# Kernel tuning notes

Hardware: AMD Instinct MI355X
Metric: run time of the kernel (lower is better)

## Reference

```python
import jax, jax.numpy as jnp
import numpy as np

N, E, IN, HID, OUT, L = 50000, 800000, 128, 64, 40, 3


def setup_inputs() -> dict:
    key = jax.random.key(0)
    ks = jax.random.split(key, 10)
    x = jax.random.normal(ks[0], (N, IN), jnp.float32)
    edge_index = jax.random.randint(ks[1], (2, E), 0, N, dtype=jnp.int32)

    def u(k, shape, fan_in):
        s = 1.0 / np.sqrt(fan_in)
        return jax.random.uniform(k, shape, jnp.float32, -s, s)

    return {
        "x": x,
        "edge_index": edge_index,
        # former1 (NWGformerF): in -> hidden projection
        "Wf": u(ks[2], (IN, HID), IN),
        "bf": jnp.zeros((HID,), jnp.float32),
        # stacked GCNConv weights (hidden->hidden)
        "conv_W": u(ks[3], (L, HID, HID), HID),
        "conv_b": jnp.zeros((L, HID), jnp.float32),
        # residual linears
        "lin_W": u(ks[4], (L, HID, HID), HID),
        "lin_b": u(ks[5], (L, HID), HID),
        # batchnorm (eval mode: affine with running stats)
        "gamma": jnp.ones((L, HID), jnp.float32),
        "beta": jnp.zeros((L, HID), jnp.float32),
        "run_mean": jnp.zeros((L, HID), jnp.float32),
        "run_var": jnp.ones((L, HID), jnp.float32),
        # output head
        "pred_W": u(ks[6], (HID, OUT), HID),
        "pred_b": jnp.zeros((OUT,), jnp.float32),
    }


def reference(x, edge_index, Wf, bf, conv_W, conv_b, lin_W, lin_b,
              gamma, beta, run_mean, run_var, pred_W, pred_b):
    n = x.shape[0]
    src, dst = edge_index[0], edge_index[1]
    eps = 1e-5

    # GCN symmetric normalization with self-loops: deg over dst (+1 self loop)
    deg = jax.ops.segment_sum(jnp.ones(src.shape[0], x.dtype), dst,
                              num_segments=n) + 1.0
    dinv = jax.lax.rsqrt(deg)                      # [N]
    edge_coef = dinv[src] * dinv[dst]              # [E]
    self_coef = (dinv * dinv)[:, None]             # [N,1]

    def gcn(h, W, b):
        hw = h @ W                                 # [N,HID]
        agg = jax.ops.segment_sum(hw[src] * edge_coef[:, None], dst,
                                  num_segments=n)
        return agg + hw * self_coef + b

    # former1: in -> hidden (dropout is identity in eval mode)
    h = x @ Wf + bf

    for i in range(L):
        h = gcn(h, conv_W[i], conv_b[i]) + h @ lin_W[i] + lin_b[i]  # res
        h = (h - run_mean[i]) * (gamma[i] * jax.lax.rsqrt(run_var[i] + eps)) + beta[i]
        h = jax.nn.relu(h)

    return h @ pred_W + pred_b
```

## Files before the change

kernel.cpp:

```cpp
#include <hip/hip_runtime.h>
#include <hip/hip_bf16.h>
#include <hip/hip_fp16.h>

#define IN_DIM 128
#define HID 64
#define OUT_DIM 40
#define SPAD 68

typedef __hip_bfloat16 bf16;
typedef unsigned short u16;
typedef _Float16 f16;
typedef __attribute__((ext_vector_type(8))) _Float16 f16x8;
typedef __attribute__((ext_vector_type(4))) float f32x4;

__device__ __forceinline__ float b2f(bf16 v) { return __bfloat162float(v); }
__device__ __forceinline__ float relu_f(float x) { return 0.5f * (x + fabsf(x)); }
__device__ __forceinline__ float ldv(const void* p, int i, int is32) {
    return is32 ? ((const float*)p)[i] : b2f(((const bf16*)p)[i]);
}

__global__ void MPNNs_60198261620971_kernel() {}

__global__ void canary_k(float* out, int m) {
    int i = blockIdx.x * blockDim.x + threadIdx.x;
    if (i < m) out[i] = 1234.0f;
}


__global__ void zerodetect_k(unsigned int* __restrict__ c2r, int nw,
                             const unsigned int* __restrict__ rv, int* __restrict__ flag) {
    int i = blockIdx.x * blockDim.x + threadIdx.x;
    if (i < nw) c2r[i] = 0;
    if (i == 0) flag[0] = (rv[0] == 0x3F800000u) ? 1 : 0;
}

__global__ void count_k(const int* __restrict__ dst, unsigned int* __restrict__ c2r,
                        u16* __restrict__ rank, int e, int n, int n2) {
    int i = blockIdx.x * blockDim.x + threadIdx.x;
    if (i >= e) return;
    int xcc = __builtin_amdgcn_s_getreg((31u << 11) | 20) & 7;
    int d = dst[i];
    u16 r = 0;
    if ((unsigned)d < (unsigned)n) {
        int sh = (d & 1) * 16;
        unsigned old = atomicAdd(&c2r[(size_t)xcc * n2 + (d >> 1)], 1u << sh);
        r = (u16)(((old >> sh) & 0x1FFFu) | ((unsigned)xcc << 13));
    }
    rank[i] = r;
}

__global__ void scan1_k(const unsigned int* __restrict__ c2r, int* __restrict__ row_ptr,
                        int* __restrict__ psum, float* __restrict__ dinv,
                        u16* __restrict__ base, int n, int n2) {
    __shared__ int sdata[1024];
    int i = blockIdx.x * 1024 + threadIdx.x;
    int v = 0;
    if (i < n) {
        int sh = (i & 1) * 16;
        int acc = 0;
        u16 b[8];
        #pragma unroll
        for (int r = 0; r < 8; r++) {
            b[r] = (u16)acc;
            acc += (int)((c2r[(size_t)r * n2 + (i >> 1)] >> sh) & 0xFFFFu);
        }
        v = acc;
        uint4 bw;
        bw.x = (unsigned)b[0] | ((unsigned)b[1] << 16);
        bw.y = (unsigned)b[2] | ((unsigned)b[3] << 16);
        bw.z = (unsigned)b[4] | ((unsigned)b[5] << 16);
        bw.w = (unsigned)b[6] | ((unsigned)b[7] << 16);
        *(uint4*)&base[(size_t)i * 8] = bw;
        dinv[i] = rsqrtf((float)v + 1.0f);
    }
    sdata[threadIdx.x] = v;
    __syncthreads();
    for (int off = 1; off < 1024; off <<= 1) {
        int t = (threadIdx.x >= off) ? sdata[threadIdx.x - off] : 0;
        __syncthreads();
        sdata[threadIdx.x] += t;
        __syncthreads();
    }
    if (i < n) row_ptr[i] = sdata[threadIdx.x] - v;
    if (threadIdx.x == 1023) psum[blockIdx.x] = sdata[1023];
}

__global__ void scan2_k(int* __restrict__ psum, int* __restrict__ row_ptr, int nb, int n) {
    __shared__ int sdata[1024];
    int v = (threadIdx.x < nb) ? psum[threadIdx.x] : 0;
    sdata[threadIdx.x] = v;
    __syncthreads();
    for (int off = 1; off < 1024; off <<= 1) {
        int t = (threadIdx.x >= off) ? sdata[threadIdx.x - off] : 0;
        __syncthreads();
        sdata[threadIdx.x] += t;
        __syncthreads();
    }
    if (threadIdx.x < nb) psum[threadIdx.x] = sdata[threadIdx.x] - v;
    if (threadIdx.x == 1023) row_ptr[n] = sdata[1023];
}

__global__ void scan3_k(int* __restrict__ row_ptr, const int* __restrict__ psum, int n) {
    int i = blockIdx.x * blockDim.x + threadIdx.x;
    if (i < n) row_ptr[i] += psum[i >> 10];
}

__global__ void fill_k(const int* __restrict__ src, const int* __restrict__ dst,
                       const int* __restrict__ row_ptr, const u16* __restrict__ rank,
                       const u16* __restrict__ base, u16* __restrict__ col, int e, int n) {
    int i = blockIdx.x * blockDim.x + threadIdx.x;
    if (i < e) {
        int d = dst[i];
        if ((unsigned)d < (unsigned)n) {
            u16 rw = rank[i];
            int rep = rw >> 13, lr = rw & 0x1FFF;
            col[row_ptr[d] + (int)base[(size_t)d * 8 + rep] + lr] = (u16)src[i];
        }
    }
}


__global__ __launch_bounds__(256) void former_k(const void* __restrict__ x,
                                                const void* __restrict__ Wf,
                                                const void* __restrict__ bfv,
                                                const int* __restrict__ dflag,
                                                float* __restrict__ h, int n) {
    __shared__ float sW[IN_DIM * HID];
    __shared__ float sx[64 * SPAD];
    int is32 = dflag[0];
    if (is32) {
        const float4* w4 = (const float4*)Wf;
        for (int i = threadIdx.x; i < IN_DIM * HID / 4; i += 256) ((float4*)sW)[i] = w4[i];
    } else {
        for (int i = threadIdx.x; i < IN_DIM * HID; i += 256) sW[i] = b2f(((const bf16*)Wf)[i]);
    }
    int tid = threadIdx.x, cg = tid & 15, rg = tid >> 4;
    int rowBase = blockIdx.x * 64;
    float acc[4][4];
    #pragma unroll
    for (int i = 0; i < 4; i++)
        #pragma unroll
        for (int j = 0; j < 4; j++) acc[i][j] = 0.f;

    for (int p = 0; p < 2; p++) {
        __syncthreads();
        #pragma unroll
        for (int pass = 0; pass < 4; pass++) {
            int r = pass * 16 + (tid >> 4);
            int c = (tid & 15) * 4;
            int gr = rowBase + r;
            float4 v = make_float4(0.f, 0.f, 0.f, 0.f);
            if (gr < n) {
                if (is32) v = *(const float4*)((const float*)x + (size_t)gr * IN_DIM + p * 64 + c);
                else {
                    const bf16* xb = (const bf16*)x + (size_t)gr * IN_DIM + p * 64 + c;
                    v = make_float4(b2f(xb[0]), b2f(xb[1]), b2f(xb[2]), b2f(xb[3]));
                }
            }
            *(float4*)&sx[r * SPAD + c] = v;
        }
        __syncthreads();
        for (int k = 0; k < 64; k += 4) {
            float4 hr[4], w[4];
            #pragma unroll
            for (int i = 0; i < 4; i++) hr[i] = *(float4*)&sx[(rg * 4 + i) * SPAD + k];
            #pragma unroll
            for (int j = 0; j < 4; j++) w[j] = *(float4*)&sW[(p * 64 + k + j) * HID + cg * 4];
            #pragma unroll
            for (int i = 0; i < 4; i++) {
                const float* hh = (const float*)&hr[i];
                #pragma unroll
                for (int j = 0; j < 4; j++) {
                    const float* ww = (const float*)&w[j];
                    acc[i][0] += hh[j] * ww[0];
                    acc[i][1] += hh[j] * ww[1];
                    acc[i][2] += hh[j] * ww[2];
                    acc[i][3] += hh[j] * ww[3];
                }
            }
        }
    }
    float b0 = ldv(bfv, cg * 4 + 0, is32), b1 = ldv(bfv, cg * 4 + 1, is32);
    float b2 = ldv(bfv, cg * 4 + 2, is32), b3 = ldv(bfv, cg * 4 + 3, is32);
    #pragma unroll
    for (int i = 0; i < 4; i++) {
        int r = rowBase + rg * 4 + i;
        if (r < n) {
            float4 o = make_float4(acc[i][0] + b0, acc[i][1] + b1, acc[i][2] + b2, acc[i][3] + b3);
            *(float4*)&h[(size_t)r * HID + cg * 4] = o;
        }
    }
}

__global__ __launch_bounds__(256) void dense_k(float* __restrict__ h,
                                               const void* __restrict__ convW,
                                               const void* __restrict__ linW,
                                               const void* __restrict__ convB,
                                               const void* __restrict__ linB,
                                               const int* __restrict__ dflag,
                                               const float* __restrict__ dinv,
                                               __half* __restrict__ hws, int n, int l) {
    __shared__ __align__(16) f16 wT[2][HID][72];
    int is32 = dflag[0];
    int wOff = l * HID * HID, vOff = l * HID;
    for (int i = threadIdx.x; i < HID * HID; i += 256) {
        int k = i >> 6, nn = i & 63;
        wT[0][nn][k] = (f16)ldv(convW, wOff + i, is32);
        wT[1][nn][k] = (f16)ldv(linW, wOff + i, is32);
    }
    __syncthreads();
    int wave = threadIdx.x >> 6, lane = threadIdx.x & 63;
    int m = lane & 15, quad = lane >> 4;
    int row0 = blockIdx.x * 64 + wave * 16;
    if (row0 >= n) return;
    int ar = row0 + m;
    const float* hp = h + (size_t)((ar < n) ? ar : 0) * HID;
    float4 v0 = *(const float4*)(hp + quad * 8);
    float4 v1 = *(const float4*)(hp + quad * 8 + 4);
    float4 v2 = *(const float4*)(hp + 32 + quad * 8);
    float4 v3 = *(const float4*)(hp + 32 + quad * 8 + 4);
    f16x8 a0 = { (f16)v0.x, (f16)v0.y, (f16)v0.z, (f16)v0.w,
                 (f16)v1.x, (f16)v1.y, (f16)v1.z, (f16)v1.w };
    f16x8 a1 = { (f16)v2.x, (f16)v2.y, (f16)v2.z, (f16)v2.w,
                 (f16)v3.x, (f16)v3.y, (f16)v3.z, (f16)v3.w };
    f32x4 acc[2][4];
    #pragma unroll
    for (int t = 0; t < 2; t++)
        #pragma unroll
        for (int ct = 0; ct < 4; ct++) acc[t][ct] = (f32x4){0.f, 0.f, 0.f, 0.f};
    #pragma unroll
    for (int ct = 0; ct < 4; ct++) {
        int nn = ct * 16 + m;
        f16x8 b00 = *(const f16x8*)&wT[0][nn][quad * 8];
        f16x8 b01 = *(const f16x8*)&wT[0][nn][32 + quad * 8];
        f16x8 b10 = *(const f16x8*)&wT[1][nn][quad * 8];
        f16x8 b11 = *(const f16x8*)&wT[1][nn][32 + quad * 8];
        acc[0][ct] = __builtin_amdgcn_mfma_f32_16x16x32_f16(a0, b00, acc[0][ct], 0, 0, 0);
        acc[0][ct] = __builtin_amdgcn_mfma_f32_16x16x32_f16(a1, b01, acc[0][ct], 0, 0, 0);
        acc[1][ct] = __builtin_amdgcn_mfma_f32_16x16x32_f16(a0, b10, acc[1][ct], 0, 0, 0);
        acc[1][ct] = __builtin_amdgcn_mfma_f32_16x16x32_f16(a1, b11, acc[1][ct], 0, 0, 0);
    }
    float cbv[4];
    #pragma unroll
    for (int ct = 0; ct < 4; ct++)
        cbv[ct] = ldv(convB, vOff + ct * 16 + m, is32) + ldv(linB, vOff + ct * 16 + m, is32);
    #pragma unroll
    for (int r = 0; r < 4; r++) {
        int row = row0 + quad * 4 + r;
        if (row < n) {
            float dv = dinv[row];
            #pragma unroll
            for (int ct = 0; ct < 4; ct++) {
                int colx = ct * 16 + m;
                hws[(size_t)row * HID + colx] = __float2half(acc[0][ct][r] * dv);
                h[(size_t)row * HID + colx] = acc[1][ct][r] + cbv[ct];
            }
        }
    }
}

__global__ __launch_bounds__(256) void agg_k(const __half* __restrict__ hws,
                                             const float* __restrict__ dinv,
                                             const int* __restrict__ row_ptr,
                                             const u16* __restrict__ col,
                                             const void* __restrict__ gamma,
                                             const void* __restrict__ beta,
                                             const void* __restrict__ mean,
                                             const void* __restrict__ var,
                                             const int* __restrict__ dflag,
                                             float* __restrict__ h, int n, int l) {
    int gwave = (blockIdx.x * blockDim.x + threadIdx.x) >> 6;
    int lane = threadIdx.x & 63;
    int nw = (gridDim.x * blockDim.x) >> 6;
    int half = lane >> 5, c = lane & 31;
    const __half2* hws2 = (const __half2*)hws;
    int is32 = dflag[0];
    int vOff = l * HID;
    float mn0 = ldv(mean, vOff + 2 * c, is32),     mn1 = ldv(mean, vOff + 2 * c + 1, is32);
    float sc0 = ldv(gamma, vOff + 2 * c, is32) * rsqrtf(ldv(var, vOff + 2 * c, is32) + 1e-5f);
    float sc1 = ldv(gamma, vOff + 2 * c + 1, is32) * rsqrtf(ldv(var, vOff + 2 * c + 1, is32) + 1e-5f);
    float bt0 = ldv(beta, vOff + 2 * c, is32),     bt1 = ldv(beta, vOff + 2 * c + 1, is32);
    for (int v = gwave; v < n; v += nw) {
        int s0 = row_ptr[v], s1 = row_ptr[v + 1];
        float2 a[8];
        #pragma unroll
        for (int g = 0; g < 8; g++) a[g] = make_float2(0.f, 0.f);
        if (half == 0) {
            float2 s = __half22float2(hws2[(size_t)v * 32 + c]);
            a[0].x += s.x; a[0].y += s.y;
        }
        for (int j0 = s0; j0 < s1; j0 += 64) {
            int myidx = (j0 + lane < s1) ? (int)col[j0 + lane] : 0;
            int cnt = min(64, s1 - j0);
            int t = 0;
            for (; t + 16 <= cnt; t += 16) {
                #pragma unroll
                for (int g = 0; g < 8; g++) {
                    int idx = __shfl(myidx, t + 2 * g + half);
                    idx = ((unsigned)idx < (unsigned)n) ? idx : 0;
                    float2 p = __half22float2(hws2[(size_t)idx * 32 + c]);
                    a[g].x += p.x; a[g].y += p.y;
                }
            }
            for (; t < cnt; t += 2) {
                int has = (t + half) < cnt;
                int sel = t + half; if (sel >= cnt) sel = cnt - 1;
                int idx = __shfl(myidx, sel);
                idx = ((unsigned)idx < (unsigned)n) ? idx : 0;
                float2 p = __half22float2(hws2[(size_t)idx * 32 + c]);
                if (has) { a[0].x += p.x; a[0].y += p.y; }
            }
        }
        float ax = ((a[0].x + a[1].x) + (a[2].x + a[3].x)) + ((a[4].x + a[5].x) + (a[6].x + a[7].x));
        float ay = ((a[0].y + a[1].y) + (a[2].y + a[3].y)) + ((a[4].y + a[5].y) + (a[6].y + a[7].y));
        float px = __shfl(ax, c + 32);
        float py = __shfl(ay, c + 32);
        if (half == 0) {
            float dv = dinv[v];
            float2 basev = *(const float2*)&h[(size_t)v * HID + 2 * c];
            float vx = dv * (ax + px) + basev.x;
            float vy = dv * (ay + py) + basev.y;
            vx = (vx - mn0) * sc0 + bt0;
            vy = (vy - mn1) * sc1 + bt1;
            float2 o = make_float2(relu_f(vx), relu_f(vy));
            *(float2*)&h[(size_t)v * HID + 2 * c] = o;
        }
    }
}

__global__ __launch_bounds__(256) void pred_k(const float* __restrict__ h,
                                              const void* __restrict__ pW,
                                              const void* __restrict__ pb,
                                              const int* __restrict__ dflag,
                                              void* __restrict__ out, int n) {
    __shared__ float sW[HID * OUT_DIM];
    __shared__ float sh[64 * SPAD];
    int is32 = dflag[0];
    if (is32) {
        const float4* w4 = (const float4*)pW;
        for (int i = threadIdx.x; i < HID * OUT_DIM / 4; i += 256) ((float4*)sW)[i] = w4[i];
    } else {
        for (int i = threadIdx.x; i < HID * OUT_DIM; i += 256) sW[i] = b2f(((const bf16*)pW)[i]);
    }
    int tid = threadIdx.x, cg = tid & 15, rg = tid >> 4;
    int rowBase = blockIdx.x * 64;
    #pragma unroll
    for (int pass = 0; pass < 4; pass++) {
        int r = pass * 16 + (tid >> 4);
        int c = (tid & 15) * 4;
        int gr = rowBase + r;
        float4 v = (gr < n) ? *(const float4*)&h[(size_t)gr * HID + c] : make_float4(0.f, 0.f, 0.f, 0.f);
        *(float4*)&sh[r * SPAD + c] = v;
    }
    __syncthreads();
    if (cg < 10) {
        float acc[4][4];
        #pragma unroll
        for (int i = 0; i < 4; i++)
            #pragma unroll
            for (int j = 0; j < 4; j++) acc[i][j] = 0.f;
        for (int k = 0; k < 64; k += 4) {
            float4 hr[4], w[4];
            #pragma unroll
            for (int i = 0; i < 4; i++) hr[i] = *(float4*)&sh[(rg * 4 + i) * SPAD + k];
            #pragma unroll
            for (int j = 0; j < 4; j++) w[j] = *(float4*)&sW[(k + j) * OUT_DIM + cg * 4];
            #pragma unroll
            for (int i = 0; i < 4; i++) {
                const float* hh = (const float*)&hr[i];
                #pragma unroll
                for (int j = 0; j < 4; j++) {
                    const float* ww = (const float*)&w[j];
                    acc[i][0] += hh[j] * ww[0];
                    acc[i][1] += hh[j] * ww[1];
                    acc[i][2] += hh[j] * ww[2];
                    acc[i][3] += hh[j] * ww[3];
                }
            }
        }
        float b0 = ldv(pb, cg * 4 + 0, is32), b1 = ldv(pb, cg * 4 + 1, is32);
        float b2 = ldv(pb, cg * 4 + 2, is32), b3 = ldv(pb, cg * 4 + 3, is32);
        #pragma unroll
        for (int i = 0; i < 4; i++) {
            int r = rowBase + rg * 4 + i;
            if (r < n) {
                if (is32) {
                    float4 o = make_float4(acc[i][0] + b0, acc[i][1] + b1, acc[i][2] + b2, acc[i][3] + b3);
                    *(float4*)((float*)out + (size_t)r * OUT_DIM + cg * 4) = o;
                } else {
                    bf16* ob = (bf16*)out + (size_t)r * OUT_DIM + cg * 4;
                    ob[0] = __float2bfloat16(acc[i][0] + b0);
                    ob[1] = __float2bfloat16(acc[i][1] + b1);
                    ob[2] = __float2bfloat16(acc[i][2] + b2);
                    ob[3] = __float2bfloat16(acc[i][3] + b3);
                }
            }
        }
    }
}


extern "C" void kernel_launch(void* const* d_in, const int* in_sizes, int n_in,
                              void* d_out, int out_size, void* d_ws, size_t ws_size,
                              hipStream_t stream) {
    const void* x     = d_in[0];
    const int*  ei    = (const int*)d_in[1];
    const void* Wf    = d_in[2];
    const void* bfv   = d_in[3];
    const void* convW = d_in[4];
    const void* convB = d_in[5];
    const void* linW  = d_in[6];
    const void* linB  = d_in[7];
    const void* gamma = d_in[8];
    const void* beta  = d_in[9];
    const void* rmean = d_in[10];
    const void* rvar  = d_in[11];
    const void* pW    = d_in[12];
    const void* pb    = d_in[13];

    const int n = in_sizes[0] / IN_DIM;
    const int e = in_sizes[1] / 2;
    const int L = in_sizes[5] / HID;
    const int n2 = (n + 1) / 2;

    const int* src = ei;
    const int* dst = ei + e;

    char* ws = (char*)d_ws;
    size_t off = 0;
    auto take = [&](size_t bytes) {
        char* p = ws + off;
        off = (off + bytes + 255) & ~(size_t)255;
        return p;
    };
    float*        h       = (float*)take((size_t)n * HID * 4);
    __half*       hws     = (__half*)take((size_t)n * HID * 2);
    float*        dinv    = (float*)take((size_t)n * 4);
    unsigned int* c2r     = (unsigned int*)take((size_t)8 * n2 * 4);
    u16*          base    = (u16*)take((size_t)n * 8 * 2);
    int*          row_ptr = (int*)take((size_t)(n + 1) * 4);
    u16*          rank    = (u16*)take((size_t)e * 2);
    u16*          colbuf  = (u16*)take((size_t)e * 2);
    int*          psum    = (int*)take(1024 * 4);
    int*          dflag   = (int*)take(256);

    if (off > ws_size || n > 65535) {
        canary_k<<<(out_size + 255) / 256, 256, 0, stream>>>((float*)d_out, out_size);
        return;
    }

    const int eblocks = (e + 255) / 256;
    const int nblocks = (n + 255) / 256;
    const int nb1024  = (n + 1023) / 1024;
    const int nb64    = (n + 63) / 64;
    const int nwords  = 8 * n2;

    zerodetect_k<<<(nwords + 255) / 256, 256, 0, stream>>>(c2r, nwords,
                                                           (const unsigned int*)rvar, dflag);
    count_k<<<eblocks, 256, 0, stream>>>(dst, c2r, rank, e, n, n2);
    scan1_k<<<nb1024, 1024, 0, stream>>>(c2r, row_ptr, psum, dinv, base, n, n2);
    scan2_k<<<1, 1024, 0, stream>>>(psum, row_ptr, nb1024, n);
    scan3_k<<<nblocks, 256, 0, stream>>>(row_ptr, psum, n);
    fill_k<<<eblocks, 256, 0, stream>>>(src, dst, row_ptr, rank, base, colbuf, e, n);

    former_k<<<nb64, 256, 0, stream>>>(x, Wf, bfv, dflag, h, n);

    for (int l = 0; l < L; l++) {
        dense_k<<<nb64, 256, 0, stream>>>(h, convW, linW, convB, linB,
                                          dflag, dinv, hws, n, l);
        agg_k<<<2048, 256, 0, stream>>>(hws, dinv, row_ptr, colbuf,
                                        gamma, beta, rmean, rvar, dflag, h, n, l);
    }

    pred_k<<<nb64, 256, 0, stream>>>(h, pW, pb, dflag, (void*)d_out, n);
}
```

Before: 325.7 us.

## Fuse CSR build with dense kernels, drop per-XCC counters, fold pred into last agg

```diff
diff --git a/kernel.cpp b/kernel.cpp
--- a/kernel.cpp
+++ b/kernel.cpp
@@ -5,7 +5,6 @@
 #define IN_DIM 128
 #define HID 64
 #define OUT_DIM 40
-#define SPAD 68
 
 typedef __hip_bfloat16 bf16;
 typedef unsigned short u16;
@@ -27,50 +26,99 @@
 }
 
 
-__global__ void zerodetect_k(unsigned int* __restrict__ c2r, int nw,
+__global__ void zerodetect_k(unsigned int* __restrict__ c2, int n2,
                              const unsigned int* __restrict__ rv, int* __restrict__ flag) {
     int i = blockIdx.x * blockDim.x + threadIdx.x;
-    if (i < nw) c2r[i] = 0;
+    if (i < n2) c2[i] = 0;
     if (i == 0) flag[0] = (rv[0] == 0x3F800000u) ? 1 : 0;
 }
 
-__global__ void count_k(const int* __restrict__ dst, unsigned int* __restrict__ c2r,
-                        u16* __restrict__ rank, int e, int n, int n2) {
-    int i = blockIdx.x * blockDim.x + threadIdx.x;
-    if (i >= e) return;
-    int xcc = __builtin_amdgcn_s_getreg((31u << 11) | 20) & 7;
-    int d = dst[i];
-    u16 r = 0;
-    if ((unsigned)d < (unsigned)n) {
-        int sh = (d & 1) * 16;
-        unsigned old = atomicAdd(&c2r[(size_t)xcc * n2 + (d >> 1)], 1u << sh);
-        r = (u16)(((old >> sh) & 0x1FFFu) | ((unsigned)xcc << 13));
-    }
-    rank[i] = r;
-}
-
-__global__ void scan1_k(const unsigned int* __restrict__ c2r, int* __restrict__ row_ptr,
-                        int* __restrict__ psum, float* __restrict__ dinv,
-                        u16* __restrict__ base, int n, int n2) {
+__global__ __launch_bounds__(256) void cntform_k(const int* __restrict__ dst,
+                                                 unsigned int* __restrict__ c2,
+                                                 u16* __restrict__ rank, int e, int n,
+                                                 int eblocks,
+                                                 const void* __restrict__ x,
+                                                 const void* __restrict__ Wf,
+                                                 const void* __restrict__ bfv,
+                                                 const int* __restrict__ dflag,
+                                                 float* __restrict__ h) {
+    __shared__ __align__(16) f16 wT[HID][IN_DIM + 8];
+    if (blockIdx.x < eblocks) {
+        int i = blockIdx.x * 256 + threadIdx.x;
+        if (i < e) {
+            int d = dst[i];
+            u16 r = 0;
+            if ((unsigned)d < (unsigned)n) {
+                int sh = (d & 1) * 16;
+                unsigned old = atomicAdd(&c2[d >> 1], 1u << sh);
+                r = (u16)((old >> sh) & 0xFFFFu);
+            }
+            rank[i] = r;
+        }
+        return;
+    }
+    int is32 = dflag[0];
+    for (int i = threadIdx.x; i < IN_DIM * HID; i += 256) {
+        int k = i >> 6, nn = i & 63;
+        wT[nn][k] = (f16)ldv(Wf, i, is32);
+    }
+    __syncthreads();
+    int wave = threadIdx.x >> 6, lane = threadIdx.x & 63;
+    int m = lane & 15, quad = lane >> 4;
+    int row0 = (int)(blockIdx.x - eblocks) * 64 + wave * 16;
+    if (row0 >= n) return;
+    int ar = row0 + m;
+    int arc = (ar < n) ? ar : (n - 1);
+    f16x8 a[4];
+    if (is32) {
+        const float* xp = (const float*)x + (size_t)arc * IN_DIM;
+        #pragma unroll
+        for (int cn = 0; cn < 4; cn++) {
+            float4 u0 = *(const float4*)(xp + cn * 32 + quad * 8);
+            float4 u1 = *(const float4*)(xp + cn * 32 + quad * 8 + 4);
+            a[cn] = (f16x8){ (f16)u0.x, (f16)u0.y, (f16)u0.z, (f16)u0.w,
+                             (f16)u1.x, (f16)u1.y, (f16)u1.z, (f16)u1.w };
+        }
+    } else {
+        const bf16* xp = (const bf16*)x + (size_t)arc * IN_DIM;
+        #pragma unroll
+        for (int cn = 0; cn < 4; cn++)
+            #pragma unroll
+            for (int j = 0; j < 8; j++) a[cn][j] = (f16)b2f(xp[cn * 32 + quad * 8 + j]);
+    }
+    f32x4 acc[4];
+    #pragma unroll
+    for (int ct = 0; ct < 4; ct++) acc[ct] = (f32x4){0.f, 0.f, 0.f, 0.f};
+    #pragma unroll
+    for (int ct = 0; ct < 4; ct++) {
+        int nn = ct * 16 + m;
+        #pragma unroll
+        for (int cn = 0; cn < 4; cn++) {
+            f16x8 b = *(const f16x8*)&wT[nn][cn * 32 + quad * 8];
+            acc[ct] = __builtin_amdgcn_mfma_f32_16x16x32_f16(a[cn], b, acc[ct], 0, 0, 0);
+        }
+    }
+    float bias[4];
+    #pragma unroll
+    for (int ct = 0; ct < 4; ct++) bias[ct] = ldv(bfv, ct * 16 + m, is32);
+    #pragma unroll
+    for (int r = 0; r < 4; r++) {
+        int row = row0 + quad * 4 + r;
+        if (row < n) {
+            #pragma unroll
+            for (int ct = 0; ct < 4; ct++)
+                h[(size_t)row * HID + ct * 16 + m] = acc[ct][r] + bias[ct];
+        }
+    }
+}
+
+__global__ void scan1_k(const unsigned int* __restrict__ c2, int* __restrict__ row_ptr,
+                        int* __restrict__ psum, float* __restrict__ dinv, int n) {
     __shared__ int sdata[1024];
     int i = blockIdx.x * 1024 + threadIdx.x;
     int v = 0;
     if (i < n) {
-        int sh = (i & 1) * 16;
-        int acc = 0;
-        u16 b[8];
-        #pragma unroll
-        for (int r = 0; r < 8; r++) {
-            b[r] = (u16)acc;
-            acc += (int)((c2r[(size_t)r * n2 + (i >> 1)] >> sh) & 0xFFFFu);
-        }
-        v = acc;
-        uint4 bw;
-        bw.x = (unsigned)b[0] | ((unsigned)b[1] << 16);
-        bw.y = (unsigned)b[2] | ((unsigned)b[3] << 16);
-        bw.z = (unsigned)b[4] | ((unsigned)b[5] << 16);
-        bw.w = (unsigned)b[6] | ((unsigned)b[7] << 16);
-        *(uint4*)&base[(size_t)i * 8] = bw;
+        v = (int)((c2[i >> 1] >> ((i & 1) * 16)) & 0xFFFFu);
         dinv[i] = rsqrtf((float)v + 1.0f);
     }
     sdata[threadIdx.x] = v;
@@ -96,98 +144,92 @@
         sdata[threadIdx.x] += t;
         __syncthreads();
     }
-    if (threadIdx.x < nb) psum[threadIdx.x] = sdata[threadIdx.x] - v;
-    if (threadIdx.x == 1023) row_ptr[n] = sdata[1023];
-}
-
-__global__ void scan3_k(int* __restrict__ row_ptr, const int* __restrict__ psum, int n) {
-    int i = blockIdx.x * blockDim.x + threadIdx.x;
-    if (i < n) row_ptr[i] += psum[i >> 10];
-}
-
-__global__ void fill_k(const int* __restrict__ src, const int* __restrict__ dst,
-                       const int* __restrict__ row_ptr, const u16* __restrict__ rank,
-                       const u16* __restrict__ base, u16* __restrict__ col, int e, int n) {
-    int i = blockIdx.x * blockDim.x + threadIdx.x;
-    if (i < e) {
-        int d = dst[i];
-        if ((unsigned)d < (unsigned)n) {
-            u16 rw = rank[i];
-            int rep = rw >> 13, lr = rw & 0x1FFF;
-            col[row_ptr[d] + (int)base[(size_t)d * 8 + rep] + lr] = (u16)src[i];
-        }
-    }
-}
-
-
-__global__ __launch_bounds__(256) void former_k(const void* __restrict__ x,
-                                                const void* __restrict__ Wf,
-                                                const void* __restrict__ bfv,
-                                                const int* __restrict__ dflag,
-                                                float* __restrict__ h, int n) {
-    __shared__ float sW[IN_DIM * HID];
-    __shared__ float sx[64 * SPAD];
+    int excl = sdata[threadIdx.x] - v;
+    if (threadIdx.x < nb) psum[threadIdx.x] = excl;
+    int lastblk = n >> 10;
+    if (threadIdx.x == lastblk) {
+        if (lastblk >= nb) psum[lastblk] = excl;
+        row_ptr[n] = sdata[1023] - excl;
+    }
+}
+
+__global__ __launch_bounds__(256) void filldense_k(const int* __restrict__ src,
+                                                   const int* __restrict__ dst,
+                                                   const int* __restrict__ row_ptr,
+                                                   const int* __restrict__ psum,
+                                                   const u16* __restrict__ rank,
+                                                   u16* __restrict__ col, int e, int eblocks,
+                                                   float* __restrict__ h,
+                                                   const void* __restrict__ convW,
+                                                   const void* __restrict__ linW,
+                                                   const void* __restrict__ convB,
+                                                   const void* __restrict__ linB,
+                                                   const int* __restrict__ dflag,
+                                                   const float* __restrict__ dinv,
+                                                   __half* __restrict__ hws, int n) {
+    __shared__ __align__(16) f16 wT2[2][HID][72];
+    if (blockIdx.x < eblocks) {
+        int i = blockIdx.x * 256 + threadIdx.x;
+        if (i < e) {
+            int d = dst[i];
+            if ((unsigned)d < (unsigned)n)
+                col[row_ptr[d] + psum[d >> 10] + (int)rank[i]] = (u16)src[i];
+        }
+        return;
+    }
     int is32 = dflag[0];
-    if (is32) {
-        const float4* w4 = (const float4*)Wf;
-        for (int i = threadIdx.x; i < IN_DIM * HID / 4; i += 256) ((float4*)sW)[i] = w4[i];
-    } else {
-        for (int i = threadIdx.x; i < IN_DIM * HID; i += 256) sW[i] = b2f(((const bf16*)Wf)[i]);
-    }
-    int tid = threadIdx.x, cg = tid & 15, rg = tid >> 4;
-    int rowBase = blockIdx.x * 64;
-    float acc[4][4];
-    #pragma unroll
-    for (int i = 0; i < 4; i++)
-        #pragma unroll
-        for (int j = 0; j < 4; j++) acc[i][j] = 0.f;
-
-    for (int p = 0; p < 2; p++) {
-        __syncthreads();
-        #pragma unroll
-        for (int pass = 0; pass < 4; pass++) {
-            int r = pass * 16 + (tid >> 4);
-            int c = (tid & 15) * 4;
-            int gr = rowBase + r;
-            float4 v = make_float4(0.f, 0.f, 0.f, 0.f);
-            if (gr < n) {
-                if (is32) v = *(const float4*)((const float*)x + (size_t)gr * IN_DIM + p * 64 + c);
-                else {
-                    const bf16* xb = (const bf16*)x + (size_t)gr * IN_DIM + p * 64 + c;
-                    v = make_float4(b2f(xb[0]), b2f(xb[1]), b2f(xb[2]), b2f(xb[3]));
-                }
-            }
-            *(float4*)&sx[r * SPAD + c] = v;
-        }
-        __syncthreads();
-        for (int k = 0; k < 64; k += 4) {
-            float4 hr[4], w[4];
+    for (int i = threadIdx.x; i < HID * HID; i += 256) {
+        int k = i >> 6, nn = i & 63;
+        wT2[0][nn][k] = (f16)ldv(convW, i, is32);
+        wT2[1][nn][k] = (f16)ldv(linW, i, is32);
+    }
+    __syncthreads();
+    int wave = threadIdx.x >> 6, lane = threadIdx.x & 63;
+    int m = lane & 15, quad = lane >> 4;
+    int row0 = (int)(blockIdx.x - eblocks) * 64 + wave * 16;
+    if (row0 >= n) return;
+    int ar = row0 + m;
+    const float* hp = h + (size_t)((ar < n) ? ar : 0) * HID;
+    float4 v0 = *(const float4*)(hp + quad * 8);
+    float4 v1 = *(const float4*)(hp + quad * 8 + 4);
+    float4 v2 = *(const float4*)(hp + 32 + quad * 8);
+    float4 v3 = *(const float4*)(hp + 32 + quad * 8 + 4);
+    f16x8 a0 = { (f16)v0.x, (f16)v0.y, (f16)v0.z, (f16)v0.w,
+                 (f16)v1.x, (f16)v1.y, (f16)v1.z, (f16)v1.w };
+    f16x8 a1 = { (f16)v2.x, (f16)v2.y, (f16)v2.z, (f16)v2.w,
+                 (f16)v3.x, (f16)v3.y, (f16)v3.z, (f16)v3.w };
+    f32x4 acc[2][4];
+    #pragma unroll
+    for (int t = 0; t < 2; t++)
+        #pragma unroll
+        for (int ct = 0; ct < 4; ct++) acc[t][ct] = (f32x4){0.f, 0.f, 0.f, 0.f};
+    #pragma unroll
+    for (int ct = 0; ct < 4; ct++) {
+        int nn = ct * 16 + m;
+        f16x8 b00 = *(const f16x8*)&wT2[0][nn][quad * 8];
+        f16x8 b01 = *(const f16x8*)&wT2[0][nn][32 + quad * 8];
+        f16x8 b10 = *(const f16x8*)&wT2[1][nn][quad * 8];
+        f16x8 b11 = *(const f16x8*)&wT2[1][nn][32 + quad * 8];
+        acc[0][ct] = __builtin_amdgcn_mfma_f32_16x16x32_f16(a0, b00, acc[0][ct], 0, 0, 0);
+        acc[0][ct] = __builtin_amdgcn_mfma_f32_16x16x32_f16(a1, b01, acc[0][ct], 0, 0, 0);
+        acc[1][ct] = __builtin_amdgcn_mfma_f32_16x16x32_f16(a0, b10, acc[1][ct], 0, 0, 0);
+        acc[1][ct] = __builtin_amdgcn_mfma_f32_16x16x32_f16(a1, b11, acc[1][ct], 0, 0, 0);
+    }
+    float cbv[4];
+    #pragma unroll
+    for (int ct = 0; ct < 4; ct++)
+        cbv[ct] = ldv(convB, ct * 16 + m, is32) + ldv(linB, ct * 16 + m, is32);
+    #pragma unroll
+    for (int r = 0; r < 4; r++) {
+        int row = row0 + quad * 4 + r;
+        if (row < n) {
+            float dv = dinv[row];
             #pragma unroll
-            for (int i = 0; i < 4; i++) hr[i] = *(float4*)&sx[(rg * 4 + i) * SPAD + k];
-            #pragma unroll
-            for (int j = 0; j < 4; j++) w[j] = *(float4*)&sW[(p * 64 + k + j) * HID + cg * 4];
-            #pragma unroll
-            for (int i = 0; i < 4; i++) {
-                const float* hh = (const float*)&hr[i];
-                #pragma unroll
-                for (int j = 0; j < 4; j++) {
-                    const float* ww = (const float*)&w[j];
-                    acc[i][0] += hh[j] * ww[0];
-                    acc[i][1] += hh[j] * ww[1];
-                    acc[i][2] += hh[j] * ww[2];
-                    acc[i][3] += hh[j] * ww[3];
-                }
-            }
-        }
-    }
-    float b0 = ldv(bfv, cg * 4 + 0, is32), b1 = ldv(bfv, cg * 4 + 1, is32);
-    float b2 = ldv(bfv, cg * 4 + 2, is32), b3 = ldv(bfv, cg * 4 + 3, is32);
-    #pragma unroll
-    for (int i = 0; i < 4; i++) {
-        int r = rowBase + rg * 4 + i;
-        if (r < n) {
-            float4 o = make_float4(acc[i][0] + b0, acc[i][1] + b1, acc[i][2] + b2, acc[i][3] + b3);
-            *(float4*)&h[(size_t)r * HID + cg * 4] = o;
+            for (int ct = 0; ct < 4; ct++) {
+                int colx = ct * 16 + m;
+                hws[(size_t)row * HID + colx] = __float2half(acc[0][ct][r] * dv);
+                h[(size_t)row * HID + colx] = acc[1][ct][r] + cbv[ct];
+            }
         }
     }
 }
@@ -200,13 +242,13 @@
                                                const int* __restrict__ dflag,
                                                const float* __restrict__ dinv,
                                                __half* __restrict__ hws, int n, int l) {
-    __shared__ __align__(16) f16 wT[2][HID][72];
+    __shared__ __align__(16) f16 wT2[2][HID][72];
     int is32 = dflag[0];
     int wOff = l * HID * HID, vOff = l * HID;
     for (int i = threadIdx.x; i < HID * HID; i += 256) {
         int k = i >> 6, nn = i & 63;
-        wT[0][nn][k] = (f16)ldv(convW, wOff + i, is32);
-        wT[1][nn][k] = (f16)ldv(linW, wOff + i, is32);
+        wT2[0][nn][k] = (f16)ldv(convW, wOff + i, is32);
+        wT2[1][nn][k] = (f16)ldv(linW, wOff + i, is32);
     }
     __syncthreads();
     int wave = threadIdx.x >> 6, lane = threadIdx.x & 63;
@@ -231,10 +273,10 @@
     #pragma unroll
     for (int ct = 0; ct < 4; ct++) {
         int nn = ct * 16 + m;
-        f16x8 b00 = *(const f16x8*)&wT[0][nn][quad * 8];
-        f16x8 b01 = *(const f16x8*)&wT[0][nn][32 + quad * 8];
-        f16x8 b10 = *(const f16x8*)&wT[1][nn][quad * 8];
-        f16x8 b11 = *(const f16x8*)&wT[1][nn][32 + quad * 8];
+        f16x8 b00 = *(const f16x8*)&wT2[0][nn][quad * 8];
+        f16x8 b01 = *(const f16x8*)&wT2[0][nn][32 + quad * 8];
+        f16x8 b10 = *(const f16x8*)&wT2[1][nn][quad * 8];
+        f16x8 b11 = *(const f16x8*)&wT2[1][nn][32 + quad * 8];
         acc[0][ct] = __builtin_amdgcn_mfma_f32_16x16x32_f16(a0, b00, acc[0][ct], 0, 0, 0);
         acc[0][ct] = __builtin_amdgcn_mfma_f32_16x16x32_f16(a1, b01, acc[0][ct], 0, 0, 0);
         acc[1][ct] = __builtin_amdgcn_mfma_f32_16x16x32_f16(a0, b10, acc[1][ct], 0, 0, 0);
@@ -262,26 +304,38 @@
 __global__ __launch_bounds__(256) void agg_k(const __half* __restrict__ hws,
                                              const float* __restrict__ dinv,
                                              const int* __restrict__ row_ptr,
+                                             const int* __restrict__ psum,
                                              const u16* __restrict__ col,
                                              const void* __restrict__ gamma,
                                              const void* __restrict__ beta,
                                              const void* __restrict__ mean,
                                              const void* __restrict__ var,
                                              const int* __restrict__ dflag,
-                                             float* __restrict__ h, int n, int l) {
+                                             float* __restrict__ h, int n, int l,
+                                             int dopred,
+                                             const void* __restrict__ pW,
+                                             const void* __restrict__ pb,
+                                             void* __restrict__ out) {
+    __shared__ float sWp[HID * OUT_DIM];
+    int is32 = dflag[0];
+    if (dopred) {
+        for (int i = threadIdx.x; i < HID * OUT_DIM; i += 256) sWp[i] = ldv(pW, i, is32);
+        __syncthreads();
+    }
     int gwave = (blockIdx.x * blockDim.x + threadIdx.x) >> 6;
     int lane = threadIdx.x & 63;
     int nw = (gridDim.x * blockDim.x) >> 6;
     int half = lane >> 5, c = lane & 31;
     const __half2* hws2 = (const __half2*)hws;
-    int is32 = dflag[0];
     int vOff = l * HID;
     float mn0 = ldv(mean, vOff + 2 * c, is32),     mn1 = ldv(mean, vOff + 2 * c + 1, is32);
     float sc0 = ldv(gamma, vOff + 2 * c, is32) * rsqrtf(ldv(var, vOff + 2 * c, is32) + 1e-5f);
     float sc1 = ldv(gamma, vOff + 2 * c + 1, is32) * rsqrtf(ldv(var, vOff + 2 * c + 1, is32) + 1e-5f);
     float bt0 = ldv(beta, vOff + 2 * c, is32),     bt1 = ldv(beta, vOff + 2 * c + 1, is32);
+    float pbias = (dopred && lane < OUT_DIM) ? ldv(pb, lane, is32) : 0.f;
     for (int v = gwave; v < n; v += nw) {
-        int s0 = row_ptr[v], s1 = row_ptr[v + 1];
+        int s0 = row_ptr[v] + psum[v >> 10];
+        int s1 = row_ptr[v + 1] + psum[(v + 1) >> 10];
         float2 a[8];
         #pragma unroll
         for (int g = 0; g < 8; g++) a[g] = make_float2(0.f, 0.f);
@@ -315,85 +369,30 @@
         float ay = ((a[0].y + a[1].y) + (a[2].y + a[3].y)) + ((a[4].y + a[5].y) + (a[6].y + a[7].y));
         float px = __shfl(ax, c + 32);
         float py = __shfl(ay, c + 32);
+        float vx = 0.f, vy = 0.f;
         if (half == 0) {
             float dv = dinv[v];
             float2 basev = *(const float2*)&h[(size_t)v * HID + 2 * c];
-            float vx = dv * (ax + px) + basev.x;
-            float vy = dv * (ay + py) + basev.y;
-            vx = (vx - mn0) * sc0 + bt0;
-            vy = (vy - mn1) * sc1 + bt1;
-            float2 o = make_float2(relu_f(vx), relu_f(vy));
-            *(float2*)&h[(size_t)v * HID + 2 * c] = o;
-        }
-    }
-}
-
-__global__ __launch_bounds__(256) void pred_k(const float* __restrict__ h,
-                                              const void* __restrict__ pW,
-                                              const void* __restrict__ pb,
-                                              const int* __restrict__ dflag,
-                                              void* __restrict__ out, int n) {
-    __shared__ float sW[HID * OUT_DIM];
-    __shared__ float sh[64 * SPAD];
-    int is32 = dflag[0];
-    if (is32) {
-        const float4* w4 = (const float4*)pW;
-        for (int i = threadIdx.x; i < HID * OUT_DIM / 4; i += 256) ((float4*)sW)[i] = w4[i];
-    } else {
-        for (int i = threadIdx.x; i < HID * OUT_DIM; i += 256) sW[i] = b2f(((const bf16*)pW)[i]);
-    }
-    int tid = threadIdx.x, cg = tid & 15, rg = tid >> 4;
-    int rowBase = blockIdx.x * 64;
-    #pragma unroll
-    for (int pass = 0; pass < 4; pass++) {
-        int r = pass * 16 + (tid >> 4);
-        int c = (tid & 15) * 4;
-        int gr = rowBase + r;
-        float4 v = (gr < n) ? *(const float4*)&h[(size_t)gr * HID + c] : make_float4(0.f, 0.f, 0.f, 0.f);
-        *(float4*)&sh[r * SPAD + c] = v;
-    }
-    __syncthreads();
-    if (cg < 10) {
-        float acc[4][4];
-        #pragma unroll
-        for (int i = 0; i < 4; i++)
-            #pragma unroll
-            for (int j = 0; j < 4; j++) acc[i][j] = 0.f;
-        for (int k = 0; k < 64; k += 4) {
-            float4 hr[4], w[4];
-            #pragma unroll
-            for (int i = 0; i < 4; i++) hr[i] = *(float4*)&sh[(rg * 4 + i) * SPAD + k];
-            #pragma unroll
-            for (int j = 0; j < 4; j++) w[j] = *(float4*)&sW[(k + j) * OUT_DIM + cg * 4];
-            #pragma unroll
-            for (int i = 0; i < 4; i++) {
-                const float* hh = (const float*)&hr[i];
-                #pragma unroll
-                for (int j = 0; j < 4; j++) {
-                    const float* ww = (const float*)&w[j];
-                    acc[i][0] += hh[j] * ww[0];
-                    acc[i][1] += hh[j] * ww[1];
-                    acc[i][2] += hh[j] * ww[2];
-                    acc[i][3] += hh[j] * ww[3];
-                }
-            }
-        }
-        float b0 = ldv(pb, cg * 4 + 0, is32), b1 = ldv(pb, cg * 4 + 1, is32);
-        float b2 = ldv(pb, cg * 4 + 2, is32), b3 = ldv(pb, cg * 4 + 3, is32);
-        #pragma unroll
-        for (int i = 0; i < 4; i++) {
-            int r = rowBase + rg * 4 + i;
-            if (r < n) {
-                if (is32) {
-                    float4 o = make_float4(acc[i][0] + b0, acc[i][1] + b1, acc[i][2] + b2, acc[i][3] + b3);
-                    *(float4*)((float*)out + (size_t)r * OUT_DIM + cg * 4) = o;
-                } else {
-                    bf16* ob = (bf16*)out + (size_t)r * OUT_DIM + cg * 4;
-                    ob[0] = __float2bfloat16(acc[i][0] + b0);
-                    ob[1] = __float2bfloat16(acc[i][1] + b1);
-                    ob[2] = __float2bfloat16(acc[i][2] + b2);
-                    ob[3] = __float2bfloat16(acc[i][3] + b3);
-                }
+            vx = dv * (ax + px) + basev.x;
+            vy = dv * (ay + py) + basev.y;
+            vx = relu_f((vx - mn0) * sc0 + bt0);
+            vy = relu_f((vy - mn1) * sc1 + bt1);
+        }
+        if (!dopred) {
+            if (half == 0) *(float2*)&h[(size_t)v * HID + 2 * c] = make_float2(vx, vy);
+        } else {
+            float accp = pbias;
+            #pragma unroll 8
+            for (int k2 = 0; k2 < 32; k2++) {
+                float hx = __shfl(vx, k2);
+                float hy = __shfl(vy, k2);
+                if (lane < OUT_DIM)
+                    accp += hx * sWp[(2 * k2) * OUT_DIM + lane]
+                          + hy * sWp[(2 * k2 + 1) * OUT_DIM + lane];
+            }
+            if (lane < OUT_DIM) {
+                if (is32) ((float*)out)[(size_t)v * OUT_DIM + lane] = accp;
+                else      ((bf16*)out)[(size_t)v * OUT_DIM + lane] = __float2bfloat16(accp);
             }
         }
     }
@@ -436,8 +435,7 @@
     float*        h       = (float*)take((size_t)n * HID * 4);
     __half*       hws     = (__half*)take((size_t)n * HID * 2);
     float*        dinv    = (float*)take((size_t)n * 4);
-    unsigned int* c2r     = (unsigned int*)take((size_t)8 * n2 * 4);
-    u16*          base    = (u16*)take((size_t)n * 8 * 2);
+    unsigned int* c2      = (unsigned int*)take((size_t)n2 * 4);
     int*          row_ptr = (int*)take((size_t)(n + 1) * 4);
     u16*          rank    = (u16*)take((size_t)e * 2);
     u16*          colbuf  = (u16*)take((size_t)e * 2);
@@ -450,27 +448,23 @@
     }
 
     const int eblocks = (e + 255) / 256;
-    const int nblocks = (n + 255) / 256;
     const int nb1024  = (n + 1023) / 1024;
     const int nb64    = (n + 63) / 64;
-    const int nwords  = 8 * n2;
-
-    zerodetect_k<<<(nwords + 255) / 256, 256, 0, stream>>>(c2r, nwords,
-                                                           (const unsigned int*)rvar, dflag);
-    count_k<<<eblocks, 256, 0, stream>>>(dst, c2r, rank, e, n, n2);
-    scan1_k<<<nb1024, 1024, 0, stream>>>(c2r, row_ptr, psum, dinv, base, n, n2);
+
+    zerodetect_k<<<(n2 + 255) / 256, 256, 0, stream>>>(c2, n2, (const unsigned int*)rvar, dflag);
+    cntform_k<<<eblocks + nb64, 256, 0, stream>>>(dst, c2, rank, e, n, eblocks,
+                                                  x, Wf, bfv, dflag, h);
+    scan1_k<<<nb1024, 1024, 0, stream>>>(c2, row_ptr, psum, dinv, n);
     scan2_k<<<1, 1024, 0, stream>>>(psum, row_ptr, nb1024, n);
-    scan3_k<<<nblocks, 256, 0, stream>>>(row_ptr, psum, n);
-    fill_k<<<eblocks, 256, 0, stream>>>(src, dst, row_ptr, rank, base, colbuf, e, n);
-
-    former_k<<<nb64, 256, 0, stream>>>(x, Wf, bfv, dflag, h, n);
-
+    filldense_k<<<eblocks + nb64, 256, 0, stream>>>(src, dst, row_ptr, psum, rank, colbuf,
+                                                    e, eblocks, h, convW, linW, convB, linB,
+                                                    dflag, dinv, hws, n);
     for (int l = 0; l < L; l++) {
-        dense_k<<<nb64, 256, 0, stream>>>(h, convW, linW, convB, linB,
-                                          dflag, dinv, hws, n, l);
-        agg_k<<<2048, 256, 0, stream>>>(hws, dinv, row_ptr, colbuf,
-                                        gamma, beta, rmean, rvar, dflag, h, n, l);
-    }
-
-    pred_k<<<nb64, 256, 0, stream>>>(h, pW, pb, dflag, (void*)d_out, n);
-}
+        if (l > 0)
+            dense_k<<<nb64, 256, 0, stream>>>(h, convW, linW, convB, linB,
+                                              dflag, dinv, hws, n, l);
+        agg_k<<<2048, 256, 0, stream>>>(hws, dinv, row_ptr, psum, colbuf,
+                                        gamma, beta, rmean, rvar, dflag, h, n, l,
+                                        (l == L - 1) ? 1 : 0, pW, pb, d_out);
+    }
+}
```

After: 379.8 us. 1.17x slower.
